# Kernel optimization log

Hardware: AMD Instinct MI355X
Metric: run time of the kernel (lower is better)

Reference implementation:

```python
import jax, jax.numpy as jnp
import numpy as np
from jax import lax

EPS = 1e-5


def maxpool3x3(x):
    # 3x3 max pool, stride 1, pad 1 (NCHW)
    return lax.reduce_window(x, -jnp.inf, lax.max,
                             window_dimensions=(1, 1, 3, 3),
                             window_strides=(1, 1, 1, 1),
                             padding=((0, 0), (0, 0), (1, 1), (1, 1)))


def focus_downsample(x):
    B, C, H, W = x.shape
    pad_h = (3 - H % 3) % 3
    pad_w = (3 - W % 3) % 3
    if pad_h or pad_w:
        x = jnp.pad(x, ((0, 0), (0, 0), (0, pad_h), (0, pad_w)))
    return jnp.concatenate([x[..., i::3, j::3] for i in range(3) for j in range(3)], axis=1)


def batchnorm(x, gamma, beta):
    # training-mode BatchNorm2d: stats over (B,H,W)
    mean = jnp.mean(x, axis=(0, 2, 3), keepdims=True)
    var = jnp.var(x, axis=(0, 2, 3), keepdims=True)
    g = gamma.reshape(1, -1, 1, 1)
    b = beta.reshape(1, -1, 1, 1)
    return (x - mean) * jax.lax.rsqrt(var + EPS) * g + b


def dwconv(x, w, pad_h, pad_w):
    # depthwise conv, w: (C,1,kh,kw)
    return lax.conv_general_dilated(x, w, window_strides=(1, 1),
                                    padding=((pad_h, pad_h), (pad_w, pad_w)),
                                    dimension_numbers=('NCHW', 'OIHW', 'NCHW'),
                                    feature_group_count=x.shape[1])


def h_transform(x):
    B, C, H, W = x.shape
    x = jnp.pad(x, ((0, 0), (0, 0), (0, 0), (0, W)))
    x = x.reshape(B, C, -1)[..., :-W]
    return x.reshape(B, C, H, 2 * W - 1)


def inv_h_transform(x):
    B, C, H, _ = x.shape
    x = x.reshape(B, C, -1)
    x = jnp.pad(x, ((0, 0), (0, 0), (0, H)))
    x = x.reshape(B, C, H, 2 * H)
    return x[..., :H]


def v_transform(x):
    return h_transform(x.transpose(0, 1, 3, 2)).transpose(0, 1, 3, 2)


def inv_v_transform(x):
    return inv_h_transform(x.transpose(0, 1, 3, 2)).transpose(0, 1, 3, 2)


def pixel_shuffle3(x):
    B, C9, h, w = x.shape
    C = C9 // 9
    x = x.reshape(B, C, 3, 3, h, w)
    x = x.transpose(0, 1, 4, 2, 5, 3)  # B,C,h,3,w,3
    return x.reshape(B, C, 3 * h, 3 * w)


def setup_inputs() -> dict:
    key = jax.random.key(0)
    ks = jax.random.split(key, 10)
    C, K = 64, 11
    B, H, W = 16, 144, 144
    s = 0.05
    return {
        'x': jax.random.normal(ks[0], (B, C, H, W), jnp.float32),
        'w_mixer': jax.random.normal(ks[1], (9, C, C), jnp.float32) * s,
        'g_mnorm': jnp.ones((9 * C,), jnp.float32),
        'b_mnorm': jnp.zeros((9 * C,), jnp.float32),
        'w_h1': jax.random.normal(ks[2], (C, 1, K, 3), jnp.float32) * s,
        'w_v1': jax.random.normal(ks[3], (C, 1, 3, K), jnp.float32) * s,
        'w_h2': jax.random.normal(ks[4], (C, 1, K, 3), jnp.float32) * s,
        'w_v2': jax.random.normal(ks[5], (C, 1, 3, K), jnp.float32) * s,
        'g_norm': jnp.ones((C,), jnp.float32),
        'b_norm': jnp.zeros((C,), jnp.float32),
    }


def reference(x, w_mixer, g_mnorm, b_mnorm, w_h1, w_v1, w_h2, w_v2, g_norm, b_norm):
    C = w_h1.shape[0]
    K = w_h1.shape[2]
    pad = K // 2
    H, W = x.shape[-2:]

    x_pool = maxpool3x3(x)
    x_focus = focus_downsample(x_pool)               # (B,9C,H/3,W/3)

    # grouped 1x1 conv, groups=9
    B, _, h, w = x_focus.shape
    xg = x_focus.reshape(B, 9, C, h, w)
    x_mixed = jnp.einsum('goi,bgihw->bgohw', w_mixer, xg).reshape(B, 9 * C, h, w)
    x_mixed = batchnorm(x_mixed, g_mnorm, b_mnorm)

    x_tem, x_key = x_mixed[:, :C], x_mixed[:, C:]

    x_h1 = dwconv(x_tem, w_h1, pad, 1)
    x_w1 = dwconv(x_tem, w_v1, 1, pad)
    x_h2 = inv_h_transform(dwconv(h_transform(x_tem), w_h2, pad, 1))
    x_w2 = inv_v_transform(dwconv(v_transform(x_tem), w_v2, 1, pad))

    att_map = batchnorm(x_h1 + x_w1 + x_h2 + x_w2, g_norm, b_norm)
    final_features = jnp.concatenate([att_map, x_key], axis=1)
    att = pixel_shuffle3(final_features)[..., :H, :W]
    return x * jax.nn.sigmoid(att)
```

## Files before the change

### kernel.cpp

```cpp
#include <hip/hip_runtime.h>
#include <hip/hip_bf16.h>

typedef __hip_bfloat16 bf16;
typedef unsigned short us;
typedef __attribute__((ext_vector_type(8))) short short8;
typedef __attribute__((ext_vector_type(4))) float floatx4;

__device__ __forceinline__ float b2f(bf16 v){ return __bfloat162float(v); }
__device__ __forceinline__ bf16  f2b(float v){ return __float2bfloat16(v); }
__device__ __forceinline__ float ldx(const void* p, size_t i, int isf){
    return isf ? ((const float*)p)[i] : b2f(((const bf16*)p)[i]);
}
__device__ __forceinline__ us bfbits(float v){
    bf16 h = f2b(v); return *(us*)&h;
}
__device__ __forceinline__ float us2f(us u){
    unsigned int w = ((unsigned int)u)<<16; float f; __builtin_memcpy(&f,&w,4); return f;
}

#define BB   16
#define CC   64
#define HH   144
#define WW   144
#define HS   48
#define SP   (HS*HS)
#define NTOT (BB*CC*HH*WW)
#define NCH  36864

__global__ void k_sniff(const unsigned int* __restrict__ x, int* __restrict__ flag){
    __shared__ int hit;
    if(threadIdx.x==0) hit = 0;
    __syncthreads();
    int local = 0;
    for(int t=threadIdx.x; t<4096; t+=256){
        unsigned int w = x[t];
        if(((w>>7)&0xFFu)==0xFFu || ((w>>23)&0xFFu)==0xFFu) local = 1;
    }
    if(local) atomicOr(&hit, 1);
    __syncthreads();
    if(threadIdx.x==0) *flag = hit;
}

__global__ void k_zero(float* __restrict__ p){
    for(int i=threadIdx.x; i<1280; i+=256) p[i] = 0.f;
}

__global__ __launch_bounds__(256) void k_pool3(const void* __restrict__ x,
                                               us* __restrict__ pf,
                                               const int* __restrict__ flag){
    __shared__ float l [18*148];
    __shared__ float hm[18*148];
    int isf = *flag;
    int bid = blockIdx.x;
    int strip = bid % 9;
    int bc = bid / 9;
    int b = bc>>6, c = bc&63;
    int r0 = strip*16;
    size_t base = (size_t)bc*HH*WW;
    int tid = threadIdx.x;
    for(int t=tid; t<18*18; t+=256){
        int row = t/18, ch = t%18;
        int rr = r0-1+row; int c0 = ch*8;
        float v[8];
        if(rr>=0 && rr<HH){
            if(isf){
                const float* xp = (const float*)x + base + (size_t)rr*WW + c0;
                float4 f0 = *(const float4*)xp;
                float4 f1 = *(const float4*)(xp+4);
                v[0]=f0.x;v[1]=f0.y;v[2]=f0.z;v[3]=f0.w;
                v[4]=f1.x;v[5]=f1.y;v[6]=f1.z;v[7]=f1.w;
            } else {
                const us* xp = (const us*)x + base + (size_t)rr*WW + c0;
                uint4 d = *(const uint4*)xp;
                const us* u = (const us*)&d;
                #pragma unroll
                for(int e=0;e<8;++e) v[e] = us2f(u[e]);
            }
        } else {
            #pragma unroll
            for(int e=0;e<8;++e) v[e] = -INFINITY;
        }
        #pragma unroll
        for(int e=0;e<8;++e) l[row*148 + c0 + e] = v[e];
    }
    __syncthreads();
    for(int t=tid; t<18*144; t+=256){
        int row = t/144, cc = t%144;
        float a = l[row*148+cc];
        float bb = (cc>0)   ? l[row*148+cc-1] : -INFINITY;
        float cv = (cc<143) ? l[row*148+cc+1] : -INFINITY;
        hm[row*148+cc] = fmaxf(a, fmaxf(bb,cv));
    }
    __syncthreads();
    for(int t=tid; t<576; t+=256){
        int row = t/36;
        int gj  = (t/12)%3;
        int xg  = t%12;
        int R = r0+row;
        int gi = R%3, y = R/3;
        union { us u[4]; uint2 v; } pk;
        #pragma unroll
        for(int e=0;e<4;++e){
            int xx = xg*4+e; int C = 3*xx+gj;
            float m = fmaxf(hm[row*148+C],
                      fmaxf(hm[(row+1)*148+C], hm[(row+2)*148+C]));
            pk.u[e] = bfbits(m);
        }
        size_t o = ((((size_t)(b*3+gi)*3+gj)*64 + c)*48 + y)*48 + xg*4;
        *(uint2*)&pf[o] = pk.v;
    }
}

__global__ __launch_bounds__(256) void k_mix3(const us* __restrict__ pf,
        const void* __restrict__ wmix, us* __restrict__ mixed,
        float* __restrict__ sum1, float* __restrict__ ss1,
        const int* __restrict__ flag){
    __shared__ __align__(16) us sW[4096];
    __shared__ __align__(16) us sI[288*64];
    __shared__ float sS[64], sQ[64];
    int isf = *flag;
    int bid = blockIdx.x;
    int chunk = bid%8, g = (bid/8)%9, b = bid/72;
    int gi = g/3, gj = g%3;
    int tid = threadIdx.x, lane = tid&63, w = tid>>6;
    {
        int o  = tid>>2;
        int i0 = (tid&3)*16;
        #pragma unroll
        for(int e=0;e<16;++e){
            int i = i0+e;
            float v = ldx(wmix, (size_t)g*4096 + (size_t)o*64 + i, isf);
            sW[o*64 + ((((i>>3)+o)&7)<<3) + (i&7)] = bfbits(v);
        }
    }
    if(tid<64){ sS[tid]=0.f; sQ[tid]=0.f; }
    {
        int i = lane;
        const us* src = pf + ((((size_t)(b*3+gi)*3+gj)*64 + i)*48 + (size_t)chunk*6)*48;
        for(int vv=w*9; vv<(w+1)*9; ++vv){
            uint4 d = *(const uint4*)(src + vv*8);
            const us* u = (const us*)&d;
            #pragma unroll
            for(int e=0;e<8;++e){
                int s = vv*8+e;
                sI[s*64 + ((((i>>3)+s)&7)<<3) + (i&7)] = u[e];
            }
        }
    }
    __syncthreads();
    int n = lane&15, quad = lane>>4;
    int m = w*16 + n;
    short8 a0 = *(const short8*)&sW[m*64 + (((quad     + m)&7)<<3)];
    short8 a1 = *(const short8*)&sW[m*64 + ((((4+quad) + m)&7)<<3)];
    floatx4 acc[18];
    #pragma unroll
    for(int nt=0; nt<18; ++nt) acc[nt] = (floatx4){0.f,0.f,0.f,0.f};
    #pragma unroll
    for(int nt=0; nt<18; ++nt){
        int site = nt*16 + n;
        short8 b0 = *(const short8*)&sI[site*64 + (((quad     + site)&7)<<3)];
        short8 b1 = *(const short8*)&sI[site*64 + ((((4+quad) + site)&7)<<3)];
        acc[nt] = __builtin_amdgcn_mfma_f32_16x16x32_bf16(a0, b0, acc[nt], 0,0,0);
        acc[nt] = __builtin_amdgcn_mfma_f32_16x16x32_bf16(a1, b1, acc[nt], 0,0,0);
    }
    size_t obase = (size_t)(b*576 + g*64)*SP + (size_t)chunk*288;
    float s[4] = {0,0,0,0}, q[4] = {0,0,0,0};
    #pragma unroll
    for(int nt=0; nt<18; ++nt){
        #pragma unroll
        for(int r=0;r<4;++r){
            float v = acc[nt][r];
            int o = w*16 + quad*4 + r;
            mixed[obase + (size_t)o*SP + nt*16 + n] = bfbits(v);
            s[r] += v; q[r] += v*v;
        }
    }
    #pragma unroll
    for(int off=1; off<=8; off<<=1){
        #pragma unroll
        for(int r=0;r<4;++r){
            s[r] += __shfl_xor(s[r], off, 64);
            q[r] += __shfl_xor(q[r], off, 64);
        }
    }
    if(n==0){
        #pragma unroll
        for(int r=0;r<4;++r){
            atomicAdd(&sS[w*16+quad*4+r], s[r]);
            atomicAdd(&sQ[w*16+quad*4+r], q[r]);
        }
    }
    __syncthreads();
    if(tid<64){
        atomicAdd(&sum1[g*64+tid], sS[tid]);
        atomicAdd(&ss1 [g*64+tid], sQ[tid]);
    }
}

__global__ void k_finstats(float* __restrict__ sum, float* __restrict__ ss, int C){
    int t = blockIdx.x*256 + threadIdx.x;
    if(t < C){
        float m = sum[t]/(float)NCH;
        float v = ss[t]/(float)NCH - m*m;
        sum[t] = m;
        ss[t]  = rsqrtf(v + 1e-5f);
    }
}

__global__ __launch_bounds__(256) void k_conv3(const us* __restrict__ mixed,
    const float* __restrict__ mean1, const float* __restrict__ istd1,
    const void* __restrict__ gm, const void* __restrict__ bm,
    const void* __restrict__ wh1, const void* __restrict__ wv1,
    const void* __restrict__ wh2, const void* __restrict__ wv2,
    us* __restrict__ att, float* __restrict__ sum2, float* __restrict__ ss2,
    const int* __restrict__ flag){
    __shared__ float tile[60*60];
    __shared__ float wt[4*33];
    __shared__ float r1[256], r2[256];
    int isf = *flag;
    int bid = blockIdx.x;
    int b = bid/64, c = bid%64;
    int tid = threadIdx.x;
    for(int t=tid; t<3600; t+=256) tile[t] = 0.f;
    if(tid < 132){
        int which = tid/33, k = tid%33;
        const void* wp = which==0?wh1:which==1?wv1:which==2?wh2:wv2;
        wt[tid] = ldx(wp, c*33 + k, isf);
    }
    __syncthreads();
    float m  = mean1[c];
    float is = istd1[c]*ldx(gm,c,isf);
    float be = ldx(bm,c,isf);
    const us* src = mixed + (size_t)(b*576 + c)*SP;
    for(int t=tid; t<288; t+=256){
        int h = t/6, w0 = (t%6)*8;
        uint4 d = *(const uint4*)(src + t*8);
        const us* u = (const us*)&d;
        #pragma unroll
        for(int e=0;e<8;++e)
            tile[(h+6)*60 + (w0+6) + e] = (us2f(u[e]) - m)*is + be;
    }
    __syncthreads();
    us* out = att + (size_t)(b*64 + c)*SP;
    float sl = 0.f, ql = 0.f;
    for(int t=tid; t<SP; t+=256){
        int h = t/48 + 6, w = t%48 + 6;
        float acc = 0.f;
        #pragma unroll
        for(int u=-5; u<=5; ++u)
            #pragma unroll
            for(int v=-1; v<=1; ++v)
                acc += wt[0*33 + (u+5)*3 + (v+1)] * tile[(h+u)*60 + (w+v)];
        #pragma unroll
        for(int u=-1; u<=1; ++u)
            #pragma unroll
            for(int v=-5; v<=5; ++v)
                acc += wt[1*33 + (u+1)*11 + (v+5)] * tile[(h+u)*60 + (w+v)];
        #pragma unroll
        for(int u=-5; u<=5; ++u)
            #pragma unroll
            for(int v=-1; v<=1; ++v)
                acc += wt[2*33 + (u+5)*3 + (v+1)] * tile[(h+u)*60 + (w+v-u)];
        #pragma unroll
        for(int u=-5; u<=5; ++u)
            #pragma unroll
            for(int v=-1; v<=1; ++v)
                acc += wt[3*33 + (v+1)*11 + (u+5)] * tile[(h+v-u)*60 + (w+u)];
        out[t] = bfbits(acc);
        sl += acc; ql += acc*acc;
    }
    r1[tid]=sl; r2[tid]=ql; __syncthreads();
    for(int o=128;o>0;o>>=1){
        if(tid<o){ r1[tid]+=r1[tid+o]; r2[tid]+=r2[tid+o]; }
        __syncthreads();
    }
    if(tid==0){
        atomicAdd(&sum2[c], r1[0]);
        atomicAdd(&ss2 [c], r2[0]);
    }
}

__global__ __launch_bounds__(256) void k_final3(const void* __restrict__ x,
    const us* __restrict__ mixed, const us* __restrict__ att,
    const void* __restrict__ gm, const void* __restrict__ bm,
    const void* __restrict__ gn, const void* __restrict__ bnb,
    const float* __restrict__ mean1, const float* __restrict__ istd1,
    const float* __restrict__ mean2, const float* __restrict__ istd2,
    void* __restrict__ out, const int* __restrict__ flag){
    __shared__ __align__(16) us sT[9*1152];
    __shared__ float scs[9], shs[9];
    int isf = *flag;
    int bid = blockIdx.x;
    int half = bid&1, c = (bid>>1)&63, b = bid>>7;
    int yy0 = half*24;
    int tid = threadIdx.x;
    if(tid < 9){
        int f = 9*c + tid;
        float sc, sh;
        if(f < 64){
            sc = istd2[f]*ldx(gn,f,isf);
            sh = ldx(bnb,f,isf) - mean2[f]*sc;
        } else {
            sc = istd1[f]*ldx(gm,f,isf);
            sh = ldx(bm,f,isf) - mean1[f]*sc;
        }
        scs[tid]=sc; shs[tid]=sh;
    }
    for(int t=tid; t<9*144; t+=256){
        int j = t/144, qq = t%144;
        int f = 9*c + j;
        const us* srcp = ((f<64) ? att   + (size_t)(b*64 +f)*SP
                                 : mixed + (size_t)(b*576+f)*SP) + yy0*48;
        ((uint4*)&sT[j*1152])[qq] = ((const uint4*)srcp)[qq];
    }
    __syncthreads();
    size_t pbase = (size_t)(b*64+c)*HH*WW;
    for(int t=tid; t<1296; t+=256){
        int Yl = t/18;
        int Xb = (t%18)*8;
        int yyl = Yl/3, r = Yl%3;
        float vo[8];
        #pragma unroll
        for(int k=0;k<8;++k){
            int X = Xb+k;
            int xx = X/3, sph = X%3;
            int j = 3*r + sph;
            float raw = us2f(sT[j*1152 + yyl*48 + xx]);
            float v = raw*scs[j] + shs[j];
            vo[k] = 1.f/(1.f + __expf(-v));
        }
        size_t off = pbase + (size_t)(yy0*3 + Yl)*WW + Xb;
        if(isf){
            const float4* xp = (const float4*)((const float*)x + off);
            float4 x0 = xp[0], x1 = xp[1];
            float4 o0, o1;
            o0.x = x0.x*vo[0]; o0.y = x0.y*vo[1]; o0.z = x0.z*vo[2]; o0.w = x0.w*vo[3];
            o1.x = x1.x*vo[4]; o1.y = x1.y*vo[5]; o1.z = x1.z*vo[6]; o1.w = x1.w*vo[7];
            float4* op = (float4*)((float*)out + off);
            op[0] = o0; op[1] = o1;
        } else {
            uint4 xr = *(const uint4*)((const us*)x + off);
            const us* xu = (const us*)&xr;
            union { us u[8]; uint4 v; } pk;
            #pragma unroll
            for(int k=0;k<8;++k)
                pk.u[k] = bfbits(us2f(xu[k])*vo[k]);
            *(uint4*)((us*)out + off) = pk.v;
        }
    }
}


extern "C" void kernel_launch(void* const* d_in, const int* in_sizes, int n_in,
                              void* d_out, int out_size, void* d_ws, size_t ws_size,
                              hipStream_t stream) {
    (void)in_sizes; (void)n_in; (void)out_size; (void)ws_size;
    const void* x    = d_in[0];
    const void* wmix = d_in[1];
    const void* gm   = d_in[2];
    const void* bm   = d_in[3];
    const void* wh1  = d_in[4];
    const void* wv1  = d_in[5];
    const void* wh2  = d_in[6];
    const void* wv2  = d_in[7];
    const void* gn   = d_in[8];
    const void* bnb  = d_in[9];

    us* pf = (us*)d_out;
    char* ws = (char*)d_ws;
    us*    mixed = (us*)   (ws + 0);
    us*    att   = (us*)   (ws + 42467328);
    float* st1a  = (float*)(ws + 47185920);
    float* st1b  = (float*)(ws + 47188224);
    float* st2a  = (float*)(ws + 47190528);
    float* st2b  = (float*)(ws + 47190784);
    int*   flag  = (int*)  (ws + 47191040);

    k_sniff   <<<1, 256, 0, stream>>>((const unsigned int*)x, flag);
    k_pool3   <<<BB*CC*9, 256, 0, stream>>>(x, pf, flag);
    k_zero    <<<1, 256, 0, stream>>>(st1a);
    k_mix3    <<<BB*9*8, 256, 0, stream>>>(pf, wmix, mixed, st1a, st1b, flag);
    k_finstats<<<3, 256, 0, stream>>>(st1a, st1b, 576);
    k_conv3   <<<BB*64, 256, 0, stream>>>(mixed, st1a, st1b, gm, bm,
                                          wh1, wv1, wh2, wv2, att, st2a, st2b, flag);
    k_finstats<<<1, 64, 0, stream>>>(st2a, st2b, 64);
    k_final3  <<<BB*CC*2, 256, 0, stream>>>(x, mixed, att, gm, bm, gn, bnb,
                                            st1a, st1b, st2a, st2b, d_out, flag);
}
```

Measured before the change: 269.5 us.

## Fold stats finalization into consumers, merge init kernels, register-block strip conv

Merges the sniff and zero kernels into one init kernel and drops both finstats kernels, so conv3 and final3 compute mean and inverse std from the raw sums themselves. This cuts the launch count from eight to five. The conv kernel now gives each thread four adjacent outputs with register sliding windows. It also merges the h2 and v2 weights into one precomputed 13x3 diagonal stencil, which cuts shared-memory loads and FLOPs. The cost is more registers per thread and fewer threads active in conv (576 work items over 256 threads).

```diff
diff --git a/kernel.cpp b/kernel.cpp
--- a/kernel.cpp
+++ b/kernel.cpp
@@ -26,8 +26,11 @@
 #define SP   (HS*HS)
 #define NTOT (BB*CC*HH*WW)
 #define NCH  36864
-
-__global__ void k_sniff(const unsigned int* __restrict__ x, int* __restrict__ flag){
+#define INV_NCH (1.f/36864.f)
+
+__global__ void k_init(const unsigned int* __restrict__ x, int* __restrict__ flag,
+                       float* __restrict__ stats){
+    for(int i=threadIdx.x; i<1280; i+=256) stats[i] = 0.f;
     __shared__ int hit;
     if(threadIdx.x==0) hit = 0;
     __syncthreads();
@@ -39,10 +42,6 @@
     if(local) atomicOr(&hit, 1);
     __syncthreads();
     if(threadIdx.x==0) *flag = hit;
-}
-
-__global__ void k_zero(float* __restrict__ p){
-    for(int i=threadIdx.x; i<1280; i+=256) p[i] = 0.f;
 }
 
 __global__ __launch_bounds__(256) void k_pool3(const void* __restrict__ x,
@@ -197,40 +196,42 @@
     }
 }
 
-__global__ void k_finstats(float* __restrict__ sum, float* __restrict__ ss, int C){
-    int t = blockIdx.x*256 + threadIdx.x;
-    if(t < C){
-        float m = sum[t]/(float)NCH;
-        float v = ss[t]/(float)NCH - m*m;
-        sum[t] = m;
-        ss[t]  = rsqrtf(v + 1e-5f);
-    }
-}
-
 __global__ __launch_bounds__(256) void k_conv3(const us* __restrict__ mixed,
-    const float* __restrict__ mean1, const float* __restrict__ istd1,
+    const float* __restrict__ sum1, const float* __restrict__ ss1,
     const void* __restrict__ gm, const void* __restrict__ bm,
     const void* __restrict__ wh1, const void* __restrict__ wv1,
     const void* __restrict__ wh2, const void* __restrict__ wv2,
     us* __restrict__ att, float* __restrict__ sum2, float* __restrict__ ss2,
     const int* __restrict__ flag){
-    __shared__ float tile[60*60];
-    __shared__ float wt[4*33];
+    __shared__ float tile[60*60+4];
+    __shared__ float w1[33], w2[33], w34[39];
     __shared__ float r1[256], r2[256];
     int isf = *flag;
     int bid = blockIdx.x;
     int b = bid/64, c = bid%64;
     int tid = threadIdx.x;
-    for(int t=tid; t<3600; t+=256) tile[t] = 0.f;
-    if(tid < 132){
-        int which = tid/33, k = tid%33;
-        const void* wp = which==0?wh1:which==1?wv1:which==2?wh2:wv2;
-        wt[tid] = ldx(wp, c*33 + k, isf);
-    }
-    __syncthreads();
-    float m  = mean1[c];
-    float is = istd1[c]*ldx(gm,c,isf);
-    float be = ldx(bm,c,isf);
+    for(int t=tid; t<3604; t+=256) tile[t] = 0.f;
+    if(tid < 33){
+        w1[tid] = ldx(wh1, c*33 + tid, isf);
+    } else if(tid < 66){
+        w2[tid-33] = ldx(wv1, c*33 + (tid-33), isf);
+    } else if(tid < 105){
+        int k = tid-66;
+        int r = k/3 - 6;
+        int vo = k%3 - 1;
+        float a = 0.f;
+        if(r >= -5 && r <= 5)
+            a += ldx(wh2, c*33 + (r+5)*3 + (vo+1), isf);
+        int u = vo - r;
+        if(u >= -5 && u <= 5)
+            a += ldx(wv2, c*33 + (vo+1)*11 + (u+5), isf);
+        w34[k] = a;
+    }
+    __syncthreads();
+    float mu   = sum1[c]*INV_NCH;
+    float var  = ss1[c]*INV_NCH - mu*mu;
+    float is   = rsqrtf(var + 1e-5f)*ldx(gm,c,isf);
+    float be   = ldx(bm,c,isf);
     const us* src = mixed + (size_t)(b*576 + c)*SP;
     for(int t=tid; t<288; t+=256){
         int h = t/6, w0 = (t%6)*8;
@@ -238,36 +239,59 @@
         const us* u = (const us*)&d;
         #pragma unroll
         for(int e=0;e<8;++e)
-            tile[(h+6)*60 + (w0+6) + e] = (us2f(u[e]) - m)*is + be;
+            tile[(h+6)*60 + (w0+6) + e] = (us2f(u[e]) - mu)*is + be;
     }
     __syncthreads();
     us* out = att + (size_t)(b*64 + c)*SP;
     float sl = 0.f, ql = 0.f;
-    for(int t=tid; t<SP; t+=256){
-        int h = t/48 + 6, w = t%48 + 6;
-        float acc = 0.f;
-        #pragma unroll
-        for(int u=-5; u<=5; ++u)
-            #pragma unroll
-            for(int v=-1; v<=1; ++v)
-                acc += wt[0*33 + (u+5)*3 + (v+1)] * tile[(h+u)*60 + (w+v)];
-        #pragma unroll
-        for(int u=-1; u<=1; ++u)
-            #pragma unroll
-            for(int v=-5; v<=5; ++v)
-                acc += wt[1*33 + (u+1)*11 + (v+5)] * tile[(h+u)*60 + (w+v)];
-        #pragma unroll
-        for(int u=-5; u<=5; ++u)
-            #pragma unroll
-            for(int v=-1; v<=1; ++v)
-                acc += wt[2*33 + (u+5)*3 + (v+1)] * tile[(h+u)*60 + (w+v-u)];
-        #pragma unroll
-        for(int u=-5; u<=5; ++u)
-            #pragma unroll
-            for(int v=-1; v<=1; ++v)
-                acc += wt[3*33 + (v+1)*11 + (u+5)] * tile[(h+v-u)*60 + (w+u)];
-        out[t] = bfbits(acc);
-        sl += acc; ql += acc*acc;
+    for(int t=tid; t<576; t+=256){
+        int hh = t/12 + 6;
+        int w0 = (t%12)*4 + 6;
+        float a0=0.f, a1=0.f, a2=0.f, a3=0.f;
+        #pragma unroll
+        for(int r=-1; r<=1; ++r){
+            const float* rp = &tile[(hh+r)*60 + w0];
+            float Cw[14];
+            #pragma unroll
+            for(int j=0;j<14;++j) Cw[j] = rp[j-5];
+            #pragma unroll
+            for(int v=0;v<11;++v){
+                float wv = w2[(r+1)*11 + v];
+                a0 += wv*Cw[v];   a1 += wv*Cw[v+1];
+                a2 += wv*Cw[v+2]; a3 += wv*Cw[v+3];
+            }
+        }
+        #pragma unroll
+        for(int r=-6; r<=6; ++r){
+            const float* rp = &tile[(hh+r)*60 + w0];
+            float Aw[6];
+            #pragma unroll
+            for(int j=0;j<6;++j) Aw[j] = rp[j-1-r];
+            #pragma unroll
+            for(int v=0;v<3;++v){
+                float wv = w34[(r+6)*3 + v];
+                a0 += wv*Aw[v];   a1 += wv*Aw[v+1];
+                a2 += wv*Aw[v+2]; a3 += wv*Aw[v+3];
+            }
+            if(r >= -5 && r <= 5){
+                float Bw[6];
+                #pragma unroll
+                for(int j=0;j<6;++j) Bw[j] = rp[j-1];
+                #pragma unroll
+                for(int v=0;v<3;++v){
+                    float wv = w1[(r+5)*3 + v];
+                    a0 += wv*Bw[v];   a1 += wv*Bw[v+1];
+                    a2 += wv*Bw[v+2]; a3 += wv*Bw[v+3];
+                }
+            }
+        }
+        int o = (hh-6)*48 + (w0-6);
+        union { us u[4]; uint2 v; } pk;
+        pk.u[0]=bfbits(a0); pk.u[1]=bfbits(a1);
+        pk.u[2]=bfbits(a2); pk.u[3]=bfbits(a3);
+        *(uint2*)&out[o] = pk.v;
+        sl += a0+a1+a2+a3;
+        ql += a0*a0+a1*a1+a2*a2+a3*a3;
     }
     r1[tid]=sl; r2[tid]=ql; __syncthreads();
     for(int o=128;o>0;o>>=1){
@@ -284,8 +308,8 @@
     const us* __restrict__ mixed, const us* __restrict__ att,
     const void* __restrict__ gm, const void* __restrict__ bm,
     const void* __restrict__ gn, const void* __restrict__ bnb,
-    const float* __restrict__ mean1, const float* __restrict__ istd1,
-    const float* __restrict__ mean2, const float* __restrict__ istd2,
+    const float* __restrict__ sum1, const float* __restrict__ ss1,
+    const float* __restrict__ sum2, const float* __restrict__ ss2,
     void* __restrict__ out, const int* __restrict__ flag){
     __shared__ __align__(16) us sT[9*1152];
     __shared__ float scs[9], shs[9];
@@ -296,15 +320,14 @@
     int tid = threadIdx.x;
     if(tid < 9){
         int f = 9*c + tid;
-        float sc, sh;
-        if(f < 64){
-            sc = istd2[f]*ldx(gn,f,isf);
-            sh = ldx(bnb,f,isf) - mean2[f]*sc;
-        } else {
-            sc = istd1[f]*ldx(gm,f,isf);
-            sh = ldx(bm,f,isf) - mean1[f]*sc;
-        }
-        scs[tid]=sc; shs[tid]=sh;
+        float sraw, qraw, gg, bb2;
+        if(f < 64){ sraw = sum2[f]; qraw = ss2[f]; gg = ldx(gn,f,isf);  bb2 = ldx(bnb,f,isf); }
+        else      { sraw = sum1[f]; qraw = ss1[f]; gg = ldx(gm,f,isf);  bb2 = ldx(bm,f,isf); }
+        float mm  = sraw*INV_NCH;
+        float ist = rsqrtf(qraw*INV_NCH - mm*mm + 1e-5f);
+        float sc = ist*gg;
+        scs[tid] = sc;
+        shs[tid] = bb2 - mm*sc;
     }
     for(int t=tid; t<9*144; t+=256){
         int j = t/144, qq = t%144;
@@ -376,14 +399,11 @@
     float* st2b  = (float*)(ws + 47190784);
     int*   flag  = (int*)  (ws + 47191040);
 
-    k_sniff   <<<1, 256, 0, stream>>>((const unsigned int*)x, flag);
-    k_pool3   <<<BB*CC*9, 256, 0, stream>>>(x, pf, flag);
-    k_zero    <<<1, 256, 0, stream>>>(st1a);
-    k_mix3    <<<BB*9*8, 256, 0, stream>>>(pf, wmix, mixed, st1a, st1b, flag);
-    k_finstats<<<3, 256, 0, stream>>>(st1a, st1b, 576);
-    k_conv3   <<<BB*64, 256, 0, stream>>>(mixed, st1a, st1b, gm, bm,
-                                          wh1, wv1, wh2, wv2, att, st2a, st2b, flag);
-    k_finstats<<<1, 64, 0, stream>>>(st2a, st2b, 64);
-    k_final3  <<<BB*CC*2, 256, 0, stream>>>(x, mixed, att, gm, bm, gn, bnb,
-                                            st1a, st1b, st2a, st2b, d_out, flag);
-}
+    k_init  <<<1, 256, 0, stream>>>((const unsigned int*)x, flag, st1a);
+    k_pool3 <<<BB*CC*9, 256, 0, stream>>>(x, pf, flag);
+    k_mix3  <<<BB*9*8, 256, 0, stream>>>(pf, wmix, mixed, st1a, st1b, flag);
+    k_conv3 <<<BB*64, 256, 0, stream>>>(mixed, st1a, st1b, gm, bm,
+                                        wh1, wv1, wh2, wv2, att, st2a, st2b, flag);
+    k_final3<<<BB*CC*2, 256, 0, stream>>>(x, mixed, att, gm, bm, gn, bnb,
+                                          st1a, st1b, st2a, st2b, d_out, flag);
+}
```

Result: slower. 289.0 us (+7.3%).
